# Kernel tuning notes

Hardware: AMD Instinct MI355X
Metric: run time of the kernel (lower is better)

Reference implementation:

```python
import jax, jax.numpy as jnp
import numpy as np
from jax import lax

K = 3       # kernel_conv
STRIDE = 1
PAD = 1


def setup_inputs() -> dict:
    key = jax.random.key(0)
    ks = jax.random.split(key, 11)
    b, n, H, W = 8, 64, 128, 128
    m = 64
    kk = K * K
    return {
        "x": jax.random.normal(ks[0], (b, n, H, W), jnp.float32),
        "atw1": jax.random.uniform(ks[1], (b, kk, H, W), jnp.float32),  # sigmoid-range attention1 output
        "weight": jax.random.normal(ks[2], (m, n, K, K), jnp.float32) * 0.05,
        "a2_w1": jax.random.normal(ks[3], (kk, n), jnp.float32) * 0.1,
        "a2_b1": jax.random.normal(ks[4], (kk,), jnp.float32) * 0.1,
        "a2_w2": jax.random.normal(ks[5], (kk, kk), jnp.float32) * 0.1,
        "a2_b2": jax.random.normal(ks[6], (kk,), jnp.float32) * 0.1,
        "a3_w1": jax.random.normal(ks[7], (m, n), jnp.float32) * 0.1,
        "a3_b1": jax.random.normal(ks[8], (m,), jnp.float32) * 0.1,
        "a3_w2": jax.random.normal(ks[9], (m, m), jnp.float32) * 0.1,
        "a3_b2": jax.random.normal(ks[10], (m,), jnp.float32) * 0.1,
    }


def reference(x, atw1, weight, a2_w1, a2_b1, a2_w2, a2_b2, a3_w1, a3_b1, a3_w2, a3_b2):
    b, n, H, W = x.shape
    m = weight.shape[0]
    kk = K * K
    n_H = 1 + (H + 2 * PAD - K) // STRIDE
    n_W = 1 + (W + 2 * PAD - K) // STRIDE
    P = n_H * n_W

    # F.unfold(x, k, stride, padding): [b, n*k*k, P] with channel-major ordering (c, kh, kw)
    patches = lax.conv_general_dilated_patches(
        x, (K, K), (STRIDE, STRIDE), [(PAD, PAD), (PAD, PAD)])  # [b, n*kk, n_H, n_W]
    kx = patches.reshape(b, n, kk, P)

    # attention2: global avg pool + two 1x1 convs -> per-batch per-tap ratio [b, kk]
    g = x.mean(axis=(2, 3))                                   # [b, n]
    ratio = jax.nn.relu(g @ a2_w1.T + a2_b1) @ a2_w2.T + a2_b2  # [b, kk]

    # per-pixel per-tap weight (broadcast over input channels, as the torch repeat/view does)
    a = atw1.reshape(b, kk, P) * ratio[:, :, None]            # [b, kk, P]
    wx = kx * a[:, None, :, :]                                # [b, n, kk, P]

    # dynamic-weighted im2col matmul with static conv weight
    w = weight.reshape(m, n, kk)
    y = jnp.einsum('bctp,mct->bmp', wx, w)                    # [b, m, P]

    # attention3 bias: global avg pool + two 1x1 convs -> [b, m]
    bias = jax.nn.relu(g @ a3_w1.T + a3_b1) @ a3_w2.T + a3_b2
    y = y + bias[:, :, None]

    # F.fold with kernel 1 is a reshape back to the spatial grid
    return y.reshape(b, m, n_H, n_W)
```

## Files before the change

kernel.cpp:

```cpp
#include <hip/hip_runtime.h>

typedef __attribute__((ext_vector_type(8))) short short8;
typedef __attribute__((ext_vector_type(4))) float f32x4;

#define HH 128
#define WW 128
#define TW 16
#define TH 4
#define HALOW 18
#define HALOH 6
#define NPIX (HALOW * HALOH)
#define NA (9 * TH * TW)

typedef __attribute__((address_space(1))) const unsigned int glds_src_t;
typedef __attribute__((address_space(3))) unsigned int glds_dst_t;

__device__ inline unsigned short f2bf(float f) {
    unsigned int u = __builtin_bit_cast(unsigned int, f);
    u += 0x7fffu + ((u >> 16) & 1u);
    return (unsigned short)(u >> 16);
}

__global__ __launch_bounds__(256) void prep_kernel(
    const float* __restrict__ x, const float* __restrict__ wgt,
    unsigned short* __restrict__ xT, float* __restrict__ partials,
    unsigned short* __restrict__ W3, float* __restrict__ zpage) {
    const int id = blockIdx.x;
    const int tid = threadIdx.x;
    if (id == 0 && tid < 32) zpage[tid] = 0.f;
    {
        int i = id * 256 + tid;
        if (i < 64 * 64 * 9) {
            int j = i & 7, rest = i >> 3;
            int m = rest & 63; rest >>= 6;
            int lk = rest & 3; rest >>= 2;
            int ks = rest & 1, t = rest >> 1;
            int c = ks * 32 + lk * 8 + j;
            W3[i] = f2bf(wgt[(m * 64 + c) * 9 + t]);
        }
    }
    const int b = id & 7, pt = id >> 3;
    const int p0 = pt * 64;
    __shared__ unsigned int lt[64 * 33];
    __shared__ float red[8][32][2];

    const int px = tid & 63, cp0 = tid >> 6;
    const float* xb = x + (size_t)b * 64 * (HH * WW) + p0 + px;
    #pragma unroll
    for (int i = 0; i < 8; ++i) {
        int cp = cp0 + 4 * i;
        float v0 = xb[(size_t)(2 * cp) * (HH * WW)];
        float v1 = xb[(size_t)(2 * cp + 1) * (HH * WW)];
        lt[px * 33 + cp] = (unsigned)f2bf(v0) | ((unsigned)f2bf(v1) << 16);
    }
    __syncthreads();
    #pragma unroll
    for (int it = 0; it < 2; ++it) {
        int idx = it * 256 + tid;
        int p = idx >> 3, ch = idx & 7;
        int o = p * 33 + ch * 4;
        uint4 v = make_uint4(lt[o], lt[o + 1], lt[o + 2], lt[o + 3]);
        *(uint4*)(xT + ((size_t)(b * (HH * WW) + p0 + p) * 64 + ch * 8)) = v;
    }
    {
        int cp = tid & 31, grp = tid >> 5;
        float s0 = 0.f, s1 = 0.f;
        #pragma unroll
        for (int j2 = 0; j2 < 8; ++j2) {
            unsigned u = lt[(grp * 8 + j2) * 33 + cp];
            s0 += __builtin_bit_cast(float, u << 16);
            s1 += __builtin_bit_cast(float, u & 0xffff0000u);
        }
        red[grp][cp][0] = s0;
        red[grp][cp][1] = s1;
    }
    __syncthreads();
    if (tid < 64) {
        float s = 0.f;
        #pragma unroll
        for (int g2 = 0; g2 < 8; ++g2) s += red[g2][tid >> 1][tid & 1];
        partials[(size_t)(b * 256 + pt) * 64 + tid] = s;
    }
}

__global__ __launch_bounds__(256, 2) void main_kernel(
    const unsigned short* __restrict__ xT, const float* __restrict__ atw1,
    const unsigned short* __restrict__ W3, const float* __restrict__ partials,
    const float* __restrict__ a2w1, const float* __restrict__ a2b1,
    const float* __restrict__ a2w2, const float* __restrict__ a2b2,
    const float* __restrict__ a3w1, const float* __restrict__ a3b1,
    const float* __restrict__ a3w2, const float* __restrict__ a3b2,
    float* __restrict__ out, const float* __restrict__ zpage) {
    const int id = blockIdx.x;
    const int b = id & 7;
    const int j = id >> 3;
    const int tid = threadIdx.x;
    const int lane = tid & 63;
    const int wtile = tid >> 6;
    const int lm = lane & 15;
    const int lk = lane >> 4;

    __shared__ char xsc[2][16384];
    __shared__ float alds[2][768];
    __shared__ float rb[4][64];
    __shared__ float gs[64], h3[64], h2[12], rrs[12], bbs[64];

    const char* xbb = (const char*)(xT + (size_t)b * (HH * WW) * 64);
    const float* ab = atw1 + (size_t)b * 9 * (HH * WW);
    float* ob = out + (size_t)b * 64 * (HH * WW);
    const char* zp = (const char*)zpage;

    auto STAGE = [&](int bi, int task) {
        const int py0 = (task >> 3) * TH, px0 = (task & 7) * TW;
        #pragma unroll
        for (int i = 0; i < 4; ++i) {
            int idx = i * 256 + tid;
            int pix = idx >> 3, ch = idx & 7;
            int yy = pix / HALOW;
            int xx = pix - yy * HALOW;
            int gy = py0 + yy - 1, gx = px0 + xx - 1;
            bool ok = (pix < NPIX) && (gy >= 0) && (gy < HH) && (gx >= 0) && (gx < WW);
            const char* src = ok
                ? xbb + (((size_t)(gy * WW + gx)) << 7) + ((ch * 16) ^ ((pix & 7) << 4))
                : zp;
            char* dst = &xsc[bi][(i * 256 + wtile * 64) * 16];
            __builtin_amdgcn_global_load_lds((glds_src_t*)src, (glds_dst_t*)dst, 16, 0, 0);
        }
        #pragma unroll
        for (int i = 0; i < 3; ++i) {
            int idx = i * 256 + tid;
            int t = idx >> 6, rem = idx & 63;
            int rr = rem >> 4, cc = rem & 15;
            bool ok = idx < NA;
            const char* src = ok
                ? (const char*)(ab + (size_t)t * (HH * WW) + (py0 + rr) * WW + px0 + cc)
                : zp;
            float* dst = &alds[bi][i * 256 + wtile * 64];
            __builtin_amdgcn_global_load_lds((glds_src_t*)src, (glds_dst_t*)dst, 4, 0, 0);
        }
    };

    STAGE(0, j * 4);

    short8 wfrag[9][2];
    {
        const short8* W3v = (const short8*)W3;
        #pragma unroll
        for (int t = 0; t < 9; ++t)
            #pragma unroll
            for (int ks = 0; ks < 2; ++ks)
                wfrag[t][ks] = W3v[(((t * 2 + ks) * 4 + lk) * 64) + wtile * 16 + lm];
    }

    {
        const int t = tid & 63, is = tid >> 6;
        float s = 0.f;
        #pragma unroll 8
        for (int k = 0; k < 64; ++k)
            s += partials[(size_t)(b * 256 + is + 4 * k) * 64 + t];
        rb[is][t] = s;
        __syncthreads();
        if (tid < 64)
            gs[t] = (rb[0][t] + rb[1][t] + rb[2][t] + rb[3][t]) * (1.f / (HH * WW));
        __syncthreads();
        if (tid < 64) {
            float s3 = 0.f;
            #pragma unroll 8
            for (int i = 0; i < 64; ++i) s3 += gs[i] * a3w1[t * 64 + i];
            h3[t] = fmaxf(s3 + a3b1[t], 0.f);
            if (t < 9) {
                float s2 = 0.f;
                #pragma unroll 8
                for (int i = 0; i < 64; ++i) s2 += gs[i] * a2w1[t * 64 + i];
                h2[t] = fmaxf(s2 + a2b1[t], 0.f);
            }
        }
        __syncthreads();
        if (tid < 64) {
            float o = 0.f;
            #pragma unroll 8
            for (int i = 0; i < 64; ++i) o += h3[i] * a3w2[t * 64 + i];
            bbs[t] = o + a3b2[t];
            if (t < 9) {
                float r = 0.f;
                #pragma unroll
                for (int i = 0; i < 9; ++i) r += h2[i] * a2w2[t * 9 + i];
                rrs[t] = r + a2b2[t];
            }
        }
        __syncthreads();
    }

    float rat[9];
    #pragma unroll
    for (int t = 0; t < 9; ++t) rat[t] = rrs[t];
    float biasr[4];
    #pragma unroll
    for (int q = 0; q < 4; ++q) biasr[q] = bbs[wtile * 16 + lk * 4 + q];

    #pragma unroll 1
    for (int it = 0; it < 4; ++it) {
        if (it < 3) {
            STAGE((it + 1) & 1, j * 4 + it + 1);
            __builtin_amdgcn_sched_barrier(0);
        }

        const int task = j * 4 + it;
        const int py0 = (task >> 3) * TH, px0 = (task & 7) * TW;
        const char* xs = xsc[it & 1];
        const float* al = alds[it & 1];

        #pragma unroll
        for (int g2 = 0; g2 < 2; ++g2) {
            const int r0 = g2 * 2;
            float av[2][9];
            #pragma unroll
            for (int rr = 0; rr < 2; ++rr)
                #pragma unroll
                for (int t = 0; t < 9; ++t)
                    av[rr][t] = al[t * 64 + (r0 + rr) * 16 + lm] * rat[t];

            f32x4 yac[2];
            #pragma unroll
            for (int rr = 0; rr < 2; ++rr) yac[rr] = (f32x4){0.f, 0.f, 0.f, 0.f};

            #pragma unroll
            for (int hl = 0; hl < 4; ++hl) {
                const int pixr = (r0 + hl) * HALOW + lm;
                short8 bf[3][2];
                #pragma unroll
                for (int dx = 0; dx < 3; ++dx) {
                    const int pix = pixr + dx;
                    const int sw = (pix & 7) << 4;
                    const char* bp2 = xs + pix * 128;
                    #pragma unroll
                    for (int ks = 0; ks < 2; ++ks)
                        bf[dx][ks] = __builtin_bit_cast(short8,
                            *(const uint4*)(bp2 + ((ks * 64 + lk * 16) ^ sw)));
                }
                #pragma unroll
                for (int dy = 0; dy < 3; ++dy) {
                    const int r = hl - dy;
                    if (r < 0 || r > 1) continue;
                    #pragma unroll
                    for (int dx = 0; dx < 3; ++dx) {
                        const int t = dy * 3 + dx;
                        f32x4 z = {0.f, 0.f, 0.f, 0.f};
                        z = __builtin_amdgcn_mfma_f32_16x16x32_bf16(wfrag[t][0], bf[dx][0], z, 0, 0, 0);
                        z = __builtin_amdgcn_mfma_f32_16x16x32_bf16(wfrag[t][1], bf[dx][1], z, 0, 0, 0);
                        #pragma unroll
                        for (int q = 0; q < 4; ++q) yac[r][q] = fmaf(av[r][t], z[q], yac[r][q]);
                    }
                }
            }
            #pragma unroll
            for (int rr = 0; rr < 2; ++rr) {
                const int pyg = py0 + r0 + rr;
                #pragma unroll
                for (int q = 0; q < 4; ++q) {
                    int m = wtile * 16 + lk * 4 + q;
                    ob[((size_t)m * HH + pyg) * WW + px0 + lm] = yac[rr][q] + biasr[q];
                }
            }
        }

        if (it < 3) {
            asm volatile("s_waitcnt vmcnt(16)" ::: "memory");
            __builtin_amdgcn_s_barrier();
            __builtin_amdgcn_sched_barrier(0);
        }
    }
}

extern "C" void kernel_launch(void* const* d_in, const int* in_sizes, int n_in,
                              void* d_out, int out_size, void* d_ws, size_t ws_size,
                              hipStream_t stream) {
    const float* x    = (const float*)d_in[0];
    const float* atw1 = (const float*)d_in[1];
    const float* wgt  = (const float*)d_in[2];
    const float* a2w1 = (const float*)d_in[3];
    const float* a2b1 = (const float*)d_in[4];
    const float* a2w2 = (const float*)d_in[5];
    const float* a2b2 = (const float*)d_in[6];
    const float* a3w1 = (const float*)d_in[7];
    const float* a3b1 = (const float*)d_in[8];
    const float* a3w2 = (const float*)d_in[9];
    const float* a3b2 = (const float*)d_in[10];
    float* out = (float*)d_out;

    float* ws = (float*)d_ws;
    float* zpage = ws + 640;
    unsigned short* W3 = (unsigned short*)(ws + 1024);
    float* partials = ws + 19456;
    unsigned short* xT = (unsigned short*)(ws + 150528);

    prep_kernel<<<dim3(2048), dim3(256), 0, stream>>>(x, wgt, xT, partials, W3, zpage);
    main_kernel<<<dim3(512), dim3(256), 0, stream>>>(
        xT, atw1, W3, partials, a2w1, a2b1, a2w2, a2b2,
        a3w1, a3b1, a3w2, a3b2, out, zpage);
}
```

Baseline: 37.83 us.

## Split waves across M-halves and row-halves to reuse B fragments across two M tiles

Each wave now covers two 16-row M tiles and one pair of output rows, where before it covered one M tile and all four rows. Each LDS B-fragment read now feeds two MFMAs, halving the per-wave LDS traffic for x. The change doubles the weight fragments held in registers (36 short8) and doubles the accumulators, so launch bounds drop to one block per SIMD-set. That risks lower occupancy and less latency hiding.

```diff
diff --git a/kernel.cpp b/kernel.cpp
--- a/kernel.cpp
+++ b/kernel.cpp
@@ -83,7 +83,7 @@
     }
 }
 
-__global__ __launch_bounds__(256, 2) void main_kernel(
+__global__ __launch_bounds__(256, 1) void main_kernel(
     const unsigned short* __restrict__ xT, const float* __restrict__ atw1,
     const unsigned short* __restrict__ W3, const float* __restrict__ partials,
     const float* __restrict__ a2w1, const float* __restrict__ a2b1,
@@ -96,7 +96,9 @@
     const int j = id >> 3;
     const int tid = threadIdx.x;
     const int lane = tid & 63;
-    const int wtile = tid >> 6;
+    const int w = tid >> 6;
+    const int mh = w >> 1;
+    const int rh = w & 1;
     const int lm = lane & 15;
     const int lk = lane >> 4;
 
@@ -123,7 +125,7 @@
             const char* src = ok
                 ? xbb + (((size_t)(gy * WW + gx)) << 7) + ((ch * 16) ^ ((pix & 7) << 4))
                 : zp;
-            char* dst = &xsc[bi][(i * 256 + wtile * 64) * 16];
+            char* dst = &xsc[bi][(i * 256 + w * 64) * 16];
             __builtin_amdgcn_global_load_lds((glds_src_t*)src, (glds_dst_t*)dst, 16, 0, 0);
         }
         #pragma unroll
@@ -135,21 +137,24 @@
             const char* src = ok
                 ? (const char*)(ab + (size_t)t * (HH * WW) + (py0 + rr) * WW + px0 + cc)
                 : zp;
-            float* dst = &alds[bi][i * 256 + wtile * 64];
+            float* dst = &alds[bi][i * 256 + w * 64];
             __builtin_amdgcn_global_load_lds((glds_src_t*)src, (glds_dst_t*)dst, 4, 0, 0);
         }
     };
 
     STAGE(0, j * 4);
 
-    short8 wfrag[9][2];
+    short8 wfrag[9][2][2];
     {
         const short8* W3v = (const short8*)W3;
         #pragma unroll
         for (int t = 0; t < 9; ++t)
             #pragma unroll
             for (int ks = 0; ks < 2; ++ks)
-                wfrag[t][ks] = W3v[(((t * 2 + ks) * 4 + lk) * 64) + wtile * 16 + lm];
+                #pragma unroll
+                for (int mt = 0; mt < 2; ++mt)
+                    wfrag[t][ks][mt] =
+                        W3v[(((t * 2 + ks) * 4 + lk) * 64) + (mh * 2 + mt) * 16 + lm];
     }
 
     {
@@ -194,9 +199,12 @@
     float rat[9];
     #pragma unroll
     for (int t = 0; t < 9; ++t) rat[t] = rrs[t];
-    float biasr[4];
+    float biasr[2][4];
     #pragma unroll
-    for (int q = 0; q < 4; ++q) biasr[q] = bbs[wtile * 16 + lk * 4 + q];
+    for (int mt = 0; mt < 2; ++mt)
+        #pragma unroll
+        for (int q = 0; q < 4; ++q)
+            biasr[mt][q] = bbs[(mh * 2 + mt) * 16 + lk * 4 + q];
 
     #pragma unroll 1
     for (int it = 0; it < 4; ++it) {
@@ -210,58 +218,65 @@
         const char* xs = xsc[it & 1];
         const float* al = alds[it & 1];
 
-        #pragma unroll
-        for (int g2 = 0; g2 < 2; ++g2) {
-            const int r0 = g2 * 2;
-            float av[2][9];
-            #pragma unroll
-            for (int rr = 0; rr < 2; ++rr)
-                #pragma unroll
-                for (int t = 0; t < 9; ++t)
-                    av[rr][t] = al[t * 64 + (r0 + rr) * 16 + lm] * rat[t];
-
-            f32x4 yac[2];
-            #pragma unroll
-            for (int rr = 0; rr < 2; ++rr) yac[rr] = (f32x4){0.f, 0.f, 0.f, 0.f};
-
-            #pragma unroll
-            for (int hl = 0; hl < 4; ++hl) {
-                const int pixr = (r0 + hl) * HALOW + lm;
-                short8 bf[3][2];
+        float av[2][9];
+        #pragma unroll
+        for (int r = 0; r < 2; ++r)
+            #pragma unroll
+            for (int t = 0; t < 9; ++t)
+                av[r][t] = al[t * 64 + (rh * 2 + r) * 16 + lm] * rat[t];
+
+        f32x4 yac[2][2];
+        #pragma unroll
+        for (int r = 0; r < 2; ++r)
+            #pragma unroll
+            for (int mt = 0; mt < 2; ++mt) yac[r][mt] = (f32x4){0.f, 0.f, 0.f, 0.f};
+
+        #pragma unroll
+        for (int hl = 0; hl < 4; ++hl) {
+            const int pixr = (rh * 2 + hl) * HALOW + lm;
+            short8 bf[3][2];
+            #pragma unroll
+            for (int dx = 0; dx < 3; ++dx) {
+                const int pix = pixr + dx;
+                const int sw = (pix & 7) << 4;
+                const char* bp2 = xs + pix * 128;
+                #pragma unroll
+                for (int ks = 0; ks < 2; ++ks)
+                    bf[dx][ks] = __builtin_bit_cast(short8,
+                        *(const uint4*)(bp2 + ((ks * 64 + lk * 16) ^ sw)));
+            }
+            #pragma unroll
+            for (int dy = 0; dy < 3; ++dy) {
+                const int r = hl - dy;
+                if (r < 0 || r > 1) continue;
                 #pragma unroll
                 for (int dx = 0; dx < 3; ++dx) {
-                    const int pix = pixr + dx;
-                    const int sw = (pix & 7) << 4;
-                    const char* bp2 = xs + pix * 128;
+                    const int t = dy * 3 + dx;
+                    f32x4 z0 = {0.f, 0.f, 0.f, 0.f};
+                    f32x4 z1 = {0.f, 0.f, 0.f, 0.f};
+                    z0 = __builtin_amdgcn_mfma_f32_16x16x32_bf16(wfrag[t][0][0], bf[dx][0], z0, 0, 0, 0);
+                    z0 = __builtin_amdgcn_mfma_f32_16x16x32_bf16(wfrag[t][1][0], bf[dx][1], z0, 0, 0, 0);
+                    z1 = __builtin_amdgcn_mfma_f32_16x16x32_bf16(wfrag[t][0][1], bf[dx][0], z1, 0, 0, 0);
+                    z1 = __builtin_amdgcn_mfma_f32_16x16x32_bf16(wfrag[t][1][1], bf[dx][1], z1, 0, 0, 0);
+                    const float a = av[r][t];
                     #pragma unroll
-                    for (int ks = 0; ks < 2; ++ks)
-                        bf[dx][ks] = __builtin_bit_cast(short8,
-                            *(const uint4*)(bp2 + ((ks * 64 + lk * 16) ^ sw)));
-                }
-                #pragma unroll
-                for (int dy = 0; dy < 3; ++dy) {
-                    const int r = hl - dy;
-                    if (r < 0 || r > 1) continue;
-                    #pragma unroll
-                    for (int dx = 0; dx < 3; ++dx) {
-                        const int t = dy * 3 + dx;
-                        f32x4 z = {0.f, 0.f, 0.f, 0.f};
-                        z = __builtin_amdgcn_mfma_f32_16x16x32_bf16(wfrag[t][0], bf[dx][0], z, 0, 0, 0);
-                        z = __builtin_amdgcn_mfma_f32_16x16x32_bf16(wfrag[t][1], bf[dx][1], z, 0, 0, 0);
-                        #pragma unroll
-                        for (int q = 0; q < 4; ++q) yac[r][q] = fmaf(av[r][t], z[q], yac[r][q]);
+                    for (int q = 0; q < 4; ++q) {
+                        yac[r][0][q] = fmaf(a, z0[q], yac[r][0][q]);
+                        yac[r][1][q] = fmaf(a, z1[q], yac[r][1][q]);
                     }
                 }
             }
-            #pragma unroll
-            for (int rr = 0; rr < 2; ++rr) {
-                const int pyg = py0 + r0 + rr;
+        }
+        #pragma unroll
+        for (int r = 0; r < 2; ++r) {
+            const int pyg = py0 + rh * 2 + r;
+            #pragma unroll
+            for (int mt = 0; mt < 2; ++mt)
                 #pragma unroll
                 for (int q = 0; q < 4; ++q) {
-                    int m = wtile * 16 + lk * 4 + q;
-                    ob[((size_t)m * HH + pyg) * WW + px0 + lm] = yac[rr][q] + biasr[q];
+                    int m = (mh * 2 + mt) * 16 + lk * 4 + q;
+                    ob[((size_t)m * HH + pyg) * WW + px0 + lm] = yac[r][mt][q] + biasr[mt][q];
                 }
-            }
         }
 
         if (it < 3) {
```

Result: slower. 50.22 us (+32.7%).
